# Kernel tuning notes

Measured on AMD Instinct MI355X. Metric: run time of the kernel, lower is better.

Reference implementation:

```python
import jax, jax.numpy as jnp
import numpy as np

B, T, D, I, C, H = 8192, 128, 7, 128, 10, 64
L = 2 ** D
SUBSET = int(I * 0.8)  # feature_subset_size = 102


def setup_inputs() -> dict:
    key = jax.random.key(0)
    ks = jax.random.split(key, 7)
    x = jax.random.normal(ks[0], (B, I), dtype=jnp.float32)
    # exact feature-subset mask: SUBSET ones per (tree, depth) row
    r = jax.random.uniform(ks[1], (T, D, I))
    ranks = jnp.argsort(jnp.argsort(r, axis=-1), axis=-1)
    feature_mask = (ranks < SUBSET).astype(jnp.float32)
    thresholds = jax.random.normal(ks[2], (T, D), dtype=jnp.float32)
    leaf_outputs = jax.random.normal(ks[3], (T, L, C), dtype=jnp.float32)
    W1 = jax.random.normal(ks[4], (I, H), dtype=jnp.float32) * 0.08
    b1 = jnp.zeros((H,), dtype=jnp.float32)
    W2 = jax.random.normal(ks[5], (H, T), dtype=jnp.float32) * 0.12
    b2 = jnp.zeros((T,), dtype=jnp.float32)
    return {"x": x, "feature_mask": feature_mask, "thresholds": thresholds,
            "leaf_outputs": leaf_outputs, "W1": W1, "b1": b1, "W2": W2, "b2": b2}


def reference(x, feature_mask, thresholds, leaf_outputs, W1, b1, W2, b2):
    depth = thresholds.shape[1]
    # split logits: masked feature sum minus threshold, per (batch, tree, depth)
    z = jnp.einsum('bi,tdi->btd', x, feature_mask) - thresholds[None, :, :]
    s = 0.5 * (z / (1.0 + jnp.abs(z)) + 1.0)  # scaled softsign split in (0,1)
    # probabilistic path routing: doubling concat, identical to torch loop
    p = jnp.ones((x.shape[0], feature_mask.shape[0], 1), dtype=x.dtype)
    for d in range(depth):
        sd = s[:, :, d:d + 1]            # [B, T, 1]
        p = jnp.concatenate([p * sd, p * (1.0 - sd)], axis=-1)  # [B, T, 2^(d+1)]
    leaf_probs = jax.nn.softmax(leaf_outputs, axis=-1)           # [T, L, C]
    tree_outputs = jnp.einsum('btl,tlc->btc', p, leaf_probs)     # [B, T, C]
    # instance-wise attention over trees (eval mode: no dropout)
    attn = jax.nn.softmax(jax.nn.relu(x @ W1 + b1) @ W2 + b2, axis=-1)  # [B, T]
    return jnp.sum(tree_outputs * attn[:, :, None], axis=1)     # [B, C]
```

## Files before the change

### kernel.cpp

```cpp
#include <hip/hip_runtime.h>
#include <hip/hip_bf16.h>
#include <hip/hip_fp16.h>


#define BB 8192
#define TT 128
#define II 128
#define CC 10
#define HH 64

#define OFF_SP  0
#define OFF_AT  4194304
#define OFF_LPB 4718592
#define OFF_PT  4980736

typedef __attribute__((ext_vector_type(8))) short short8;
typedef __attribute__((ext_vector_type(16))) float floatx16;

static __device__ inline unsigned int pkbf(float lo, float hi) {
  __hip_bfloat162 h = __float22bfloat162_rn(make_float2(lo, hi));
  unsigned int u;
  __builtin_memcpy(&u, &h, 4);
  return u;
}

static __device__ inline unsigned int pkh(float lo, float hi) {
  __half2 h = __float22half2_rn(make_float2(lo, hi));
  unsigned int u;
  __builtin_memcpy(&u, &h, 4);
  return u;
}

static __device__ inline short8 cvt8(float4 a, float4 b) {
  union { short8 v; unsigned int u[4]; } r;
  r.u[0] = pkbf(a.x, a.y);
  r.u[1] = pkbf(a.z, a.w);
  r.u[2] = pkbf(b.x, b.y);
  r.u[3] = pkbf(b.z, b.w);
  return r.v;
}

__global__ __launch_bounds__(256, 2) void phase1_kernel(
    const float* __restrict__ x, const float* __restrict__ mask,
    const float* __restrict__ thr, const float* __restrict__ lo,
    const float* __restrict__ W1, const float* __restrict__ b1,
    const float* __restrict__ W2, const float* __restrict__ b2,
    __half* __restrict__ sPack, __half* __restrict__ attnB,
    unsigned int* __restrict__ lpb) {
  __shared__ __align__(16) char smem_raw[32768];
  const int blk = blockIdx.x;
  const int tid = threadIdx.x;
  const int wv = tid >> 6, lane = tid & 63;
  const int half = lane >> 5, l31 = lane & 31;

  if (blk < 64) {
    const int b0 = blk * 128 + wv * 32;

    short8 axf[8];
    const float* xrow = x + (size_t)(b0 + l31) * II + half * 8;
#pragma unroll
    for (int s = 0; s < 8; ++s)
      axf[s] = cvt8(*(const float4*)(xrow + s * 16),
                    *(const float4*)(xrow + s * 16 + 4));

    floatx16 acch[2];
#pragma unroll
    for (int i = 0; i < 16; ++i) { acch[0][i] = 0.f; acch[1][i] = 0.f; }
#pragma unroll
    for (int s = 0; s < 8; ++s) {
#pragma unroll
      for (int tile = 0; tile < 2; ++tile) {
        union { short8 v; unsigned int u[4]; } wf;
#pragma unroll
        for (int jp = 0; jp < 4; ++jp) {
          int k0 = s * 16 + half * 8 + jp * 2;
          float f0 = W1[(size_t)k0 * HH + tile * 32 + l31];
          float f1 = W1[(size_t)(k0 + 1) * HH + tile * 32 + l31];
          wf.u[jp] = pkbf(f0, f1);
        }
        acch[tile] = __builtin_amdgcn_mfma_f32_32x32x16_bf16(
            axf[s], wf.v, acch[tile], 0, 0, 0);
      }
    }
    __hip_bfloat16* hids = (__hip_bfloat16*)smem_raw + wv * (32 * 72);
#pragma unroll
    for (int tile = 0; tile < 2; ++tile) {
      float bh = b1[tile * 32 + l31];
#pragma unroll
      for (int r = 0; r < 16; ++r) {
        int row = (r & 3) + 8 * (r >> 2) + 4 * half;
        hids[row * 72 + tile * 32 + l31] =
            __float2bfloat16(fmaxf(acch[tile][r] + bh, 0.f));
      }
    }
    __syncthreads();

    short8 ahf[4];
#pragma unroll
    for (int s = 0; s < 4; ++s)
      ahf[s] = *(const short8*)(hids + l31 * 72 + s * 16 + half * 8);

    floatx16 accl[4];
#pragma unroll
    for (int tile = 0; tile < 4; ++tile) {
#pragma unroll
      for (int i = 0; i < 16; ++i) accl[tile][i] = 0.f;
#pragma unroll
      for (int s = 0; s < 4; ++s) {
        union { short8 v; unsigned int u[4]; } wf;
#pragma unroll
        for (int jp = 0; jp < 4; ++jp) {
          int k0 = s * 16 + half * 8 + jp * 2;
          float f0 = W2[(size_t)k0 * TT + tile * 32 + l31];
          float f1 = W2[(size_t)(k0 + 1) * TT + tile * 32 + l31];
          wf.u[jp] = pkbf(f0, f1);
        }
        accl[tile] = __builtin_amdgcn_mfma_f32_32x32x16_bf16(
            ahf[s], wf.v, accl[tile], 0, 0, 0);
      }
      float bt = b2[tile * 32 + l31];
#pragma unroll
      for (int i = 0; i < 16; ++i) accl[tile][i] += bt;
    }

    float mrow[16];
#pragma unroll
    for (int r = 0; r < 16; ++r)
      mrow[r] = fmaxf(fmaxf(accl[0][r], accl[1][r]),
                      fmaxf(accl[2][r], accl[3][r]));
#pragma unroll
    for (int msk = 1; msk <= 16; msk <<= 1)
#pragma unroll
      for (int r = 0; r < 16; ++r)
        mrow[r] = fmaxf(mrow[r], __shfl_xor(mrow[r], msk, 64));
    float srow[16];
#pragma unroll
    for (int r = 0; r < 16; ++r) srow[r] = 0.f;
#pragma unroll
    for (int tile = 0; tile < 4; ++tile)
#pragma unroll
      for (int r = 0; r < 16; ++r) {
        float e = __expf(accl[tile][r] - mrow[r]);
        accl[tile][r] = e;
        srow[r] += e;
      }
#pragma unroll
    for (int msk = 1; msk <= 16; msk <<= 1)
#pragma unroll
      for (int r = 0; r < 16; ++r)
        srow[r] += __shfl_xor(srow[r], msk, 64);
#pragma unroll
    for (int r = 0; r < 16; ++r) srow[r] = 1.f / srow[r];

#pragma unroll
    for (int tile = 0; tile < 4; ++tile)
#pragma unroll
      for (int r = 0; r < 16; ++r) {
        int row = (r & 3) + 8 * (r >> 2) + 4 * half;
        attnB[(size_t)(b0 + row) * TT + tile * 32 + l31] =
            __float2half(accl[tile][r] * srow[r]);
      }

  } else if (blk < 576) {
    __half* lds = (__half*)smem_raw;
    const int blk2 = blk - 64;
    const int mb = blk2 >> 5;
    const int ns = blk2 & 31;
    const int m0 = mb * 56;

    short8 af0[8], af1[8];
    {
      const float* mrow0 = mask + (size_t)(m0 + l31) * II + half * 8;
      int mr1 = m0 + 28 + l31; if (mr1 > 895) mr1 = 895;
      const float* mrow1 = mask + (size_t)mr1 * II + half * 8;
#pragma unroll
      for (int s = 0; s < 8; ++s) {
        af0[s] = cvt8(*(const float4*)(mrow0 + s * 16),
                      *(const float4*)(mrow0 + s * 16 + 4));
        af1[s] = cvt8(*(const float4*)(mrow1 + s * 16),
                      *(const float4*)(mrow1 + s * 16 + 4));
      }
    }
    float th0[16], th1[16];
#pragma unroll
    for (int r = 0; r < 16; ++r) {
      int rw = (r & 3) + 8 * (r >> 2) + 4 * half;
      th0[r] = thr[m0 + rw];
      int m1 = m0 + 28 + rw;
      th1[r] = thr[m1 > 895 ? 895 : m1];
    }

#pragma unroll
    for (int nb = 0; nb < 2; ++nb) {
      const int nl = wv * 64 + nb * 32;
      const float* xrow = x + (size_t)(ns * 256 + nl + l31) * II + half * 8;
      short8 xf[8];
#pragma unroll
      for (int s = 0; s < 8; ++s)
        xf[s] = cvt8(*(const float4*)(xrow + s * 16),
                     *(const float4*)(xrow + s * 16 + 4));
      floatx16 acc0, acc1;
#pragma unroll
      for (int i = 0; i < 16; ++i) { acc0[i] = 0.f; acc1[i] = 0.f; }
#pragma unroll
      for (int s = 0; s < 8; ++s) {
        acc0 = __builtin_amdgcn_mfma_f32_32x32x16_bf16(af0[s], xf[s], acc0, 0, 0, 0);
        acc1 = __builtin_amdgcn_mfma_f32_32x32x16_bf16(af1[s], xf[s], acc1, 0, 0, 0);
      }
#pragma unroll
      for (int r = 0; r < 16; ++r) {
        int row = (r & 3) + 8 * (r >> 2) + 4 * half;
        if (row < 28) {
          int tl = row / 7;
          int d = row - tl * 7;
          float z = acc0[r] - th0[r];
          float o = 0.5f * (z / (1.f + fabsf(z)) + 1.f);
          lds[(tl * 256 + nl + l31) * 8 + d] = __float2half(o);
          z = acc1[r] - th1[r];
          o = 0.5f * (z / (1.f + fabsf(z)) + 1.f);
          lds[((tl + 4) * 256 + nl + l31) * 8 + d] = __float2half(o);
        }
      }
    }
    __syncthreads();

    const uint4* l4 = (const uint4*)lds;
#pragma unroll
    for (int j = 0; j < 8; ++j) {
      int idx = tid + 256 * j;
      ((uint4*)sPack)[(size_t)(8 * mb + (idx >> 8)) * BB + ns * 256 + (idx & 255)] =
          l4[idx];
    }

  } else {
    float* lps = (float*)smem_raw;
    const int t0 = (blk - 576) * 2;
    {
      int tl = tid >> 7, l = tid & 127;
      const float* row = lo + ((size_t)(t0 + tl) * 128 + l) * CC;
      float v[CC];
      float m = -1e30f;
#pragma unroll
      for (int c = 0; c < CC; ++c) { v[c] = row[c]; m = fmaxf(m, v[c]); }
      float s = 0.f;
#pragma unroll
      for (int c = 0; c < CC; ++c) { v[c] = __expf(v[c] - m); s += v[c]; }
      float inv = 1.f / s;
      float* o = lps + (tl * 128 + l) * 12;
#pragma unroll
      for (int c = 0; c < CC; ++c) o[c] = v[c] * inv;
      o[10] = 0.f; o[11] = 0.f;
    }
    __syncthreads();

#pragma unroll
    for (int jj = 0; jj < 4; ++jj) {
      int idx = tid + 256 * jj;
      int tl = idx >> 9, rem = idx & 511;
      int s = rem >> 6, ln = rem & 63;
      int hf = ln >> 5, n = ln & 31;
      unsigned int wd[4];
#pragma unroll
      for (int jp = 0; jp < 4; ++jp) {
        int l0 = s * 16 + hf * 8 + jp * 2;
        float f0 = (n < CC) ? lps[(tl * 128 + l0) * 12 + n] : 0.f;
        float f1 = (n < CC) ? lps[(tl * 128 + l0 + 1) * 12 + n] : 0.f;
        wd[jp] = pkh(f0, f1);
      }
      ((uint4*)lpb)[(size_t)(t0 + tl) * 512 + s * 64 + ln] =
          make_uint4(wd[0], wd[1], wd[2], wd[3]);
    }
  }
}

__global__ __launch_bounds__(256, 2) void main_kernel(
    const __half* __restrict__ sPack, const __half* __restrict__ attnB,
    const unsigned int* __restrict__ lpb, float* __restrict__ partial) {
  __shared__ float red[256 * 10];
  const int bg = blockIdx.x, tg = blockIdx.y;
  const int tid = threadIdx.x;
  const int w = tid >> 6, lane = tid & 63;
  const int half = lane >> 5;
  const int l31 = lane & 31;
  const int b0 = bg * 256 + w * 64 + l31;
  const int b1 = b0 + 32;
  const uint4* spk = (const uint4*)sPack;

  __half av0[8], av1[8];
  *(uint4*)av0 = *(const uint4*)(attnB + (size_t)b0 * TT + tg * 8);
  *(uint4*)av1 = *(const uint4*)(attnB + (size_t)b1 * TT + tg * 8);

  floatx16 acc0, acc1;
#pragma unroll
  for (int i = 0; i < 16; ++i) { acc0[i] = 0.f; acc1[i] = 0.f; }

  uint4 sv0[2], sv1[2];
  sv0[0] = spk[(size_t)(tg * 8) * BB + b0];
  sv1[0] = spk[(size_t)(tg * 8) * BB + b1];

#pragma unroll
  for (int it = 0; it < 8; ++it) {
    const int cur = it & 1;
    const int t = tg * 8 + it;
    uint4 bf[8];
    const uint4* lpt = (const uint4*)lpb + (size_t)t * 512 + lane;
#pragma unroll
    for (int s = 0; s < 8; ++s) bf[s] = lpt[s * 64];
    if (it < 7) {
      sv0[cur ^ 1] = spk[(size_t)(t + 1) * BB + b0];
      sv1[cur ^ 1] = spk[(size_t)(t + 1) * BB + b1];
    }

    __half2 pl2q[2][4];
    float wvq[2][8];
#pragma unroll
    for (int q = 0; q < 2; ++q) {
      const __half* sh = (const __half*)(q ? &sv1[cur] : &sv0[cur]);
      float s0 = __half2float(sh[0]), s1 = __half2float(sh[1]);
      float s2 = __half2float(sh[2]), s3 = __half2float(sh[3]);
      float s4 = __half2float(sh[4]), s5 = __half2float(sh[5]);
      float s6 = __half2float(sh[6]);
      float A  = __half2float(q ? av1[it] : av0[it]);

      float s0c = 1.f - s0, s1c = 1.f - s1, s2c = 1.f - s2;
      float t0 = s0 * s1, t1 = s0c * s1, t2 = s0 * s1c, t3 = s0c * s1c;
      float pl[8];
      pl[0] = t0 * s2;  pl[1] = t1 * s2;  pl[2] = t2 * s2;  pl[3] = t3 * s2;
      pl[4] = t0 * s2c; pl[5] = t1 * s2c; pl[6] = t2 * s2c; pl[7] = t3 * s2c;
      float sel3 = half ? (1.f - s3) : s3;
      float Af = A * sel3;
      float s4c = 1.f - s4, s5c = 1.f - s5;
      float as6 = Af * s6, as6c = Af * (1.f - s6);
      float u0 = s4 * s5, u1 = s4c * s5, u2 = s4 * s5c, u3 = s4c * s5c;
      wvq[q][0] = u0 * as6;  wvq[q][1] = u1 * as6;
      wvq[q][2] = u2 * as6;  wvq[q][3] = u3 * as6;
      wvq[q][4] = u0 * as6c; wvq[q][5] = u1 * as6c;
      wvq[q][6] = u2 * as6c; wvq[q][7] = u3 * as6c;
#pragma unroll
      for (int jp = 0; jp < 4; ++jp)
        pl2q[q][jp] = __float22half2_rn(make_float2(pl[jp * 2], pl[jp * 2 + 1]));
    }

#pragma unroll
    for (int s = 0; s < 8; ++s) {
      union { short8 v; __half2 h[4]; } a0, a1;
      __half2 w20 = __half2half2(__float2half(wvq[0][s]));
      __half2 w21 = __half2half2(__float2half(wvq[1][s]));
#pragma unroll
      for (int jp = 0; jp < 4; ++jp) {
        a0.h[jp] = __hmul2(pl2q[0][jp], w20);
        a1.h[jp] = __hmul2(pl2q[1][jp], w21);
      }
      acc0 = __builtin_amdgcn_mfma_f32_32x32x16_f16(
          a0.v, *(const short8*)&bf[s], acc0, 0, 0, 0);
      acc1 = __builtin_amdgcn_mfma_f32_32x32x16_f16(
          a1.v, *(const short8*)&bf[s], acc1, 0, 0, 0);
    }
  }

  const int col = l31;
  if (col < CC) {
#pragma unroll
    for (int r = 0; r < 16; ++r) {
      int row = (r & 3) + 8 * (r >> 2) + 4 * half;
      red[(w * 64 + row) * 10 + col] = acc0[r];
      red[(w * 64 + 32 + row) * 10 + col] = acc1[r];
    }
  }
  __syncthreads();
#pragma unroll
  for (int j = 0; j < 10; ++j) {
    int idx = tid + 256 * j;
    partial[(size_t)tg * 81920 + (size_t)bg * 2560 + idx] = red[idx];
  }
}

__global__ __launch_bounds__(256) void reduce_kernel(
    const float* __restrict__ partial, float* __restrict__ out) {
  int idx4 = blockIdx.x * 256 + threadIdx.x;
  float4 s = make_float4(0.f, 0.f, 0.f, 0.f);
#pragma unroll
  for (int tg = 0; tg < 16; ++tg) {
    float4 v = ((const float4*)(partial + (size_t)tg * 81920))[idx4];
    s.x += v.x; s.y += v.y; s.z += v.z; s.w += v.w;
  }
  ((float4*)out)[idx4] = s;
}

extern "C" void kernel_launch(void* const* d_in, const int* in_sizes, int n_in,
                              void* d_out, int out_size, void* d_ws, size_t ws_size,
                              hipStream_t stream) {
  const float* x    = (const float*)d_in[0];
  const float* mask = (const float*)d_in[1];
  const float* thr  = (const float*)d_in[2];
  const float* lo   = (const float*)d_in[3];
  const float* W1   = (const float*)d_in[4];
  const float* b1   = (const float*)d_in[5];
  const float* W2   = (const float*)d_in[6];
  const float* b2   = (const float*)d_in[7];
  float* out = (float*)d_out;
  float* ws  = (float*)d_ws;

  __half*       sPack   = (__half*)(ws + OFF_SP);
  __half*       attnB   = (__half*)(ws + OFF_AT);
  unsigned int* LPb     = (unsigned int*)(ws + OFF_LPB);
  float*        partial = ws + OFF_PT;

  phase1_kernel<<<640, 256, 0, stream>>>(x, mask, thr, lo, W1, b1, W2, b2,
                                         sPack, attnB, LPb);
  main_kernel<<<dim3(32, 16), 256, 0, stream>>>(sPack, attnB, LPb, partial);
  reduce_kernel<<<80, 256, 0, stream>>>(partial, out);
}
```

Baseline: 105.5 us.

## Fuse split, attention, leaf-softmax and routing into one kernel with atomic reduction

Replaces the three-kernel pipeline (phase1, main, reduce) with a single fused kernel. Each block computes its split probabilities, its slice of attention and its leaf softmaxes in LDS, then runs the routing MFMA and atomically adds its partial result into the output, which is zeroed first with a memset. This removes the workspace round trips through global memory and two kernel launches. In exchange, every block recomputes the attention MLP for its 256 rows, so that work is repeated 16 times across tree groups. LDS use also grows to about 62KB per block, which may limit occupancy, and results depend on atomic add order.

```diff
diff --git a/kernel.cpp b/kernel.cpp
--- a/kernel.cpp
+++ b/kernel.cpp
@@ -8,11 +8,6 @@
 #define II 128
 #define CC 10
 #define HH 64
-
-#define OFF_SP  0
-#define OFF_AT  4194304
-#define OFF_LPB 4718592
-#define OFF_PT  4980736
 
 typedef __attribute__((ext_vector_type(8))) short short8;
 typedef __attribute__((ext_vector_type(16))) float floatx16;
@@ -40,134 +35,23 @@
   return r.v;
 }
 
-__global__ __launch_bounds__(256, 2) void phase1_kernel(
+__global__ __launch_bounds__(256, 2) void fused_kernel(
     const float* __restrict__ x, const float* __restrict__ mask,
     const float* __restrict__ thr, const float* __restrict__ lo,
     const float* __restrict__ W1, const float* __restrict__ b1,
     const float* __restrict__ W2, const float* __restrict__ b2,
-    __half* __restrict__ sPack, __half* __restrict__ attnB,
-    unsigned int* __restrict__ lpb) {
-  __shared__ __align__(16) char smem_raw[32768];
-  const int blk = blockIdx.x;
+    float* __restrict__ out) {
+  __shared__ __align__(16) char smem_raw[63488];
   const int tid = threadIdx.x;
   const int wv = tid >> 6, lane = tid & 63;
   const int half = lane >> 5, l31 = lane & 31;
-
-  if (blk < 64) {
-    const int b0 = blk * 128 + wv * 32;
-
-    short8 axf[8];
-    const float* xrow = x + (size_t)(b0 + l31) * II + half * 8;
-#pragma unroll
-    for (int s = 0; s < 8; ++s)
-      axf[s] = cvt8(*(const float4*)(xrow + s * 16),
-                    *(const float4*)(xrow + s * 16 + 4));
-
-    floatx16 acch[2];
-#pragma unroll
-    for (int i = 0; i < 16; ++i) { acch[0][i] = 0.f; acch[1][i] = 0.f; }
-#pragma unroll
-    for (int s = 0; s < 8; ++s) {
-#pragma unroll
-      for (int tile = 0; tile < 2; ++tile) {
-        union { short8 v; unsigned int u[4]; } wf;
-#pragma unroll
-        for (int jp = 0; jp < 4; ++jp) {
-          int k0 = s * 16 + half * 8 + jp * 2;
-          float f0 = W1[(size_t)k0 * HH + tile * 32 + l31];
-          float f1 = W1[(size_t)(k0 + 1) * HH + tile * 32 + l31];
-          wf.u[jp] = pkbf(f0, f1);
-        }
-        acch[tile] = __builtin_amdgcn_mfma_f32_32x32x16_bf16(
-            axf[s], wf.v, acch[tile], 0, 0, 0);
-      }
-    }
-    __hip_bfloat16* hids = (__hip_bfloat16*)smem_raw + wv * (32 * 72);
-#pragma unroll
-    for (int tile = 0; tile < 2; ++tile) {
-      float bh = b1[tile * 32 + l31];
-#pragma unroll
-      for (int r = 0; r < 16; ++r) {
-        int row = (r & 3) + 8 * (r >> 2) + 4 * half;
-        hids[row * 72 + tile * 32 + l31] =
-            __float2bfloat16(fmaxf(acch[tile][r] + bh, 0.f));
-      }
-    }
-    __syncthreads();
-
-    short8 ahf[4];
-#pragma unroll
-    for (int s = 0; s < 4; ++s)
-      ahf[s] = *(const short8*)(hids + l31 * 72 + s * 16 + half * 8);
-
-    floatx16 accl[4];
-#pragma unroll
-    for (int tile = 0; tile < 4; ++tile) {
-#pragma unroll
-      for (int i = 0; i < 16; ++i) accl[tile][i] = 0.f;
-#pragma unroll
-      for (int s = 0; s < 4; ++s) {
-        union { short8 v; unsigned int u[4]; } wf;
-#pragma unroll
-        for (int jp = 0; jp < 4; ++jp) {
-          int k0 = s * 16 + half * 8 + jp * 2;
-          float f0 = W2[(size_t)k0 * TT + tile * 32 + l31];
-          float f1 = W2[(size_t)(k0 + 1) * TT + tile * 32 + l31];
-          wf.u[jp] = pkbf(f0, f1);
-        }
-        accl[tile] = __builtin_amdgcn_mfma_f32_32x32x16_bf16(
-            ahf[s], wf.v, accl[tile], 0, 0, 0);
-      }
-      float bt = b2[tile * 32 + l31];
-#pragma unroll
-      for (int i = 0; i < 16; ++i) accl[tile][i] += bt;
-    }
-
-    float mrow[16];
-#pragma unroll
-    for (int r = 0; r < 16; ++r)
-      mrow[r] = fmaxf(fmaxf(accl[0][r], accl[1][r]),
-                      fmaxf(accl[2][r], accl[3][r]));
-#pragma unroll
-    for (int msk = 1; msk <= 16; msk <<= 1)
-#pragma unroll
-      for (int r = 0; r < 16; ++r)
-        mrow[r] = fmaxf(mrow[r], __shfl_xor(mrow[r], msk, 64));
-    float srow[16];
-#pragma unroll
-    for (int r = 0; r < 16; ++r) srow[r] = 0.f;
-#pragma unroll
-    for (int tile = 0; tile < 4; ++tile)
-#pragma unroll
-      for (int r = 0; r < 16; ++r) {
-        float e = __expf(accl[tile][r] - mrow[r]);
-        accl[tile][r] = e;
-        srow[r] += e;
-      }
-#pragma unroll
-    for (int msk = 1; msk <= 16; msk <<= 1)
-#pragma unroll
-      for (int r = 0; r < 16; ++r)
-        srow[r] += __shfl_xor(srow[r], msk, 64);
-#pragma unroll
-    for (int r = 0; r < 16; ++r) srow[r] = 1.f / srow[r];
-
-#pragma unroll
-    for (int tile = 0; tile < 4; ++tile)
-#pragma unroll
-      for (int r = 0; r < 16; ++r) {
-        int row = (r & 3) + 8 * (r >> 2) + 4 * half;
-        attnB[(size_t)(b0 + row) * TT + tile * 32 + l31] =
-            __float2half(accl[tile][r] * srow[r]);
-      }
-
-  } else if (blk < 576) {
-    __half* lds = (__half*)smem_raw;
-    const int blk2 = blk - 64;
-    const int mb = blk2 >> 5;
-    const int ns = blk2 & 31;
-    const int m0 = mb * 56;
-
+  const int tg = blockIdx.x >> 5;
+  const int bg = blockIdx.x & 31;
+
+  __half* zsl = (__half*)smem_raw;
+
+  {
+    const int m0 = tg * 56;
     short8 af0[8], af1[8];
     {
       const float* mrow0 = mask + (size_t)(m0 + l31) * II + half * 8;
@@ -193,7 +77,7 @@
 #pragma unroll
     for (int nb = 0; nb < 2; ++nb) {
       const int nl = wv * 64 + nb * 32;
-      const float* xrow = x + (size_t)(ns * 256 + nl + l31) * II + half * 8;
+      const float* xrow = x + (size_t)(bg * 256 + nl + l31) * II + half * 8;
       short8 xf[8];
 #pragma unroll
       for (int s = 0; s < 8; ++s)
@@ -215,176 +99,264 @@
           int d = row - tl * 7;
           float z = acc0[r] - th0[r];
           float o = 0.5f * (z / (1.f + fabsf(z)) + 1.f);
-          lds[(tl * 256 + nl + l31) * 8 + d] = __float2half(o);
+          zsl[(tl * 256 + nl + l31) * 8 + d] = __float2half(o);
           z = acc1[r] - th1[r];
           o = 0.5f * (z / (1.f + fabsf(z)) + 1.f);
-          lds[((tl + 4) * 256 + nl + l31) * 8 + d] = __float2half(o);
-        }
-      }
-    }
+          zsl[((tl + 4) * 256 + nl + l31) * 8 + d] = __float2half(o);
+        }
+      }
+    }
+  }
+
+  {
+    const int tsel = tg >> 2, lsel = tg & 3;
+    __half* attnV = (__half*)(smem_raw + 59392);
+    for (int p = 0; p < 2; ++p) {
+      const int b0 = bg * 256 + p * 128 + wv * 32;
+
+      short8 axf[8];
+      const float* xrow = x + (size_t)(b0 + l31) * II + half * 8;
+#pragma unroll
+      for (int s = 0; s < 8; ++s)
+        axf[s] = cvt8(*(const float4*)(xrow + s * 16),
+                      *(const float4*)(xrow + s * 16 + 4));
+
+      floatx16 acch[2];
+#pragma unroll
+      for (int i = 0; i < 16; ++i) { acch[0][i] = 0.f; acch[1][i] = 0.f; }
+#pragma unroll
+      for (int s = 0; s < 8; ++s) {
+#pragma unroll
+        for (int tile = 0; tile < 2; ++tile) {
+          union { short8 v; unsigned int u[4]; } wf;
+#pragma unroll
+          for (int jp = 0; jp < 4; ++jp) {
+            int k0 = s * 16 + half * 8 + jp * 2;
+            float f0 = W1[(size_t)k0 * HH + tile * 32 + l31];
+            float f1 = W1[(size_t)(k0 + 1) * HH + tile * 32 + l31];
+            wf.u[jp] = pkbf(f0, f1);
+          }
+          acch[tile] = __builtin_amdgcn_mfma_f32_32x32x16_bf16(
+              axf[s], wf.v, acch[tile], 0, 0, 0);
+        }
+      }
+      __hip_bfloat16* hids = (__hip_bfloat16*)(smem_raw + 32768) + wv * (32 * 72);
+#pragma unroll
+      for (int tile = 0; tile < 2; ++tile) {
+        float bh = b1[tile * 32 + l31];
+#pragma unroll
+        for (int r = 0; r < 16; ++r) {
+          int row = (r & 3) + 8 * (r >> 2) + 4 * half;
+          hids[row * 72 + tile * 32 + l31] =
+              __float2bfloat16(fmaxf(acch[tile][r] + bh, 0.f));
+        }
+      }
+      __syncthreads();
+
+      short8 ahf[4];
+#pragma unroll
+      for (int s = 0; s < 4; ++s)
+        ahf[s] = *(const short8*)(hids + l31 * 72 + s * 16 + half * 8);
+
+      floatx16 accl[4];
+#pragma unroll
+      for (int tile = 0; tile < 4; ++tile) {
+#pragma unroll
+        for (int i = 0; i < 16; ++i) accl[tile][i] = 0.f;
+#pragma unroll
+        for (int s = 0; s < 4; ++s) {
+          union { short8 v; unsigned int u[4]; } wf;
+#pragma unroll
+          for (int jp = 0; jp < 4; ++jp) {
+            int k0 = s * 16 + half * 8 + jp * 2;
+            float f0 = W2[(size_t)k0 * TT + tile * 32 + l31];
+            float f1 = W2[(size_t)(k0 + 1) * TT + tile * 32 + l31];
+            wf.u[jp] = pkbf(f0, f1);
+          }
+          accl[tile] = __builtin_amdgcn_mfma_f32_32x32x16_bf16(
+              ahf[s], wf.v, accl[tile], 0, 0, 0);
+        }
+        float bt = b2[tile * 32 + l31];
+#pragma unroll
+        for (int i = 0; i < 16; ++i) accl[tile][i] += bt;
+      }
+
+      float mrow[16];
+#pragma unroll
+      for (int r = 0; r < 16; ++r)
+        mrow[r] = fmaxf(fmaxf(accl[0][r], accl[1][r]),
+                        fmaxf(accl[2][r], accl[3][r]));
+#pragma unroll
+      for (int msk = 1; msk <= 16; msk <<= 1)
+#pragma unroll
+        for (int r = 0; r < 16; ++r)
+          mrow[r] = fmaxf(mrow[r], __shfl_xor(mrow[r], msk, 64));
+      float srow[16];
+#pragma unroll
+      for (int r = 0; r < 16; ++r) srow[r] = 0.f;
+#pragma unroll
+      for (int tile = 0; tile < 4; ++tile)
+#pragma unroll
+        for (int r = 0; r < 16; ++r) {
+          float e = __expf(accl[tile][r] - mrow[r]);
+          accl[tile][r] = e;
+          srow[r] += e;
+        }
+#pragma unroll
+      for (int msk = 1; msk <= 16; msk <<= 1)
+#pragma unroll
+        for (int r = 0; r < 16; ++r)
+          srow[r] += __shfl_xor(srow[r], msk, 64);
+#pragma unroll
+      for (int r = 0; r < 16; ++r) srow[r] = 1.f / srow[r];
+
+#pragma unroll
+      for (int tile = 0; tile < 4; ++tile) {
+        if (tile == tsel) {
+#pragma unroll
+          for (int r = 0; r < 16; ++r) {
+            int row = (r & 3) + 8 * (r >> 2) + 4 * half;
+            if ((l31 >> 3) == lsel)
+              attnV[(p * 128 + wv * 32 + row) * 8 + (l31 & 7)] =
+                  __float2half(accl[tile][r] * srow[r]);
+          }
+        }
+      }
+      __syncthreads();
+    }
+  }
+
+  {
+    __half* lps = (__half*)(smem_raw + 53248);
+    uint4* lpB = (uint4*)(smem_raw + 32768);
+    for (int tt = 0; tt < 4; ++tt) {
+      {
+        int tl = tid >> 7, l = tid & 127;
+        const float* row = lo + ((size_t)(tg * 8 + tt * 2 + tl) * 128 + l) * CC;
+        float v[CC];
+        float m = -1e30f;
+#pragma unroll
+        for (int c = 0; c < CC; ++c) { v[c] = row[c]; m = fmaxf(m, v[c]); }
+        float s = 0.f;
+#pragma unroll
+        for (int c = 0; c < CC; ++c) { v[c] = __expf(v[c] - m); s += v[c]; }
+        float inv = 1.f / s;
+        __half* o = lps + (tl * 128 + l) * 12;
+#pragma unroll
+        for (int c = 0; c < CC; ++c) o[c] = __float2half(v[c] * inv);
+      }
+      __syncthreads();
+#pragma unroll
+      for (int jj = 0; jj < 4; ++jj) {
+        int idx = tid + 256 * jj;
+        int tl = idx >> 9, rem = idx & 511;
+        int s = rem >> 6, ln = rem & 63;
+        int hf = ln >> 5, n = ln & 31;
+        if (n < CC) {
+          unsigned int wd[4];
+#pragma unroll
+          for (int jp = 0; jp < 4; ++jp) {
+            int l0 = s * 16 + hf * 8 + jp * 2;
+            float f0 = __half2float(lps[(tl * 128 + l0) * 12 + n]);
+            float f1 = __half2float(lps[(tl * 128 + l0 + 1) * 12 + n]);
+            wd[jp] = pkh(f0, f1);
+          }
+          lpB[((tt * 2 + tl) * 8 + s) * 20 + n * 2 + hf] =
+              make_uint4(wd[0], wd[1], wd[2], wd[3]);
+        }
+      }
+      __syncthreads();
+    }
+  }
+
+  {
+    const uint4* zsl4 = (const uint4*)smem_raw;
+    const uint4* lpB = (const uint4*)(smem_raw + 32768);
+    const uint4* aV = (const uint4*)(smem_raw + 59392);
+    const int bl = wv * 64 + l31;
+
+    __half av0[8], av1[8];
+    *(uint4*)av0 = aV[bl];
+    *(uint4*)av1 = aV[bl + 32];
+
+    floatx16 acc0, acc1;
+#pragma unroll
+    for (int i = 0; i < 16; ++i) { acc0[i] = 0.f; acc1[i] = 0.f; }
+
+#pragma unroll
+    for (int it = 0; it < 8; ++it) {
+      uint4 sv0 = zsl4[it * 256 + bl];
+      uint4 sv1 = zsl4[it * 256 + bl + 32];
+      uint4 bf[8];
+#pragma unroll
+      for (int s = 0; s < 8; ++s)
+        bf[s] = (l31 < CC) ? lpB[(it * 8 + s) * 20 + l31 * 2 + half]
+                           : make_uint4(0u, 0u, 0u, 0u);
+
+      __half2 pl2q[2][4];
+      float wvq[2][8];
+#pragma unroll
+      for (int q = 0; q < 2; ++q) {
+        const __half* sh = (const __half*)(q ? &sv1 : &sv0);
+        float s0 = __half2float(sh[0]), s1 = __half2float(sh[1]);
+        float s2 = __half2float(sh[2]), s3 = __half2float(sh[3]);
+        float s4 = __half2float(sh[4]), s5 = __half2float(sh[5]);
+        float s6 = __half2float(sh[6]);
+        float A  = __half2float(q ? av1[it] : av0[it]);
+
+        float s0c = 1.f - s0, s1c = 1.f - s1, s2c = 1.f - s2;
+        float t0 = s0 * s1, t1 = s0c * s1, t2 = s0 * s1c, t3 = s0c * s1c;
+        float pl[8];
+        pl[0] = t0 * s2;  pl[1] = t1 * s2;  pl[2] = t2 * s2;  pl[3] = t3 * s2;
+        pl[4] = t0 * s2c; pl[5] = t1 * s2c; pl[6] = t2 * s2c; pl[7] = t3 * s2c;
+        float sel3 = half ? (1.f - s3) : s3;
+        float Af = A * sel3;
+        float s4c = 1.f - s4, s5c = 1.f - s5;
+        float as6 = Af * s6, as6c = Af * (1.f - s6);
+        float u0 = s4 * s5, u1 = s4c * s5, u2 = s4 * s5c, u3 = s4c * s5c;
+        wvq[q][0] = u0 * as6;  wvq[q][1] = u1 * as6;
+        wvq[q][2] = u2 * as6;  wvq[q][3] = u3 * as6;
+        wvq[q][4] = u0 * as6c; wvq[q][5] = u1 * as6c;
+        wvq[q][6] = u2 * as6c; wvq[q][7] = u3 * as6c;
+#pragma unroll
+        for (int jp = 0; jp < 4; ++jp)
+          pl2q[q][jp] = __float22half2_rn(make_float2(pl[jp * 2], pl[jp * 2 + 1]));
+      }
+
+#pragma unroll
+      for (int s = 0; s < 8; ++s) {
+        union { short8 v; __half2 h[4]; } a0, a1;
+        __half2 w20 = __half2half2(__float2half(wvq[0][s]));
+        __half2 w21 = __half2half2(__float2half(wvq[1][s]));
+#pragma unroll
+        for (int jp = 0; jp < 4; ++jp) {
+          a0.h[jp] = __hmul2(pl2q[0][jp], w20);
+          a1.h[jp] = __hmul2(pl2q[1][jp], w21);
+        }
+        acc0 = __builtin_amdgcn_mfma_f32_32x32x16_f16(
+            a0.v, *(const short8*)&bf[s], acc0, 0, 0, 0);
+        acc1 = __builtin_amdgcn_mfma_f32_32x32x16_f16(
+            a1.v, *(const short8*)&bf[s], acc1, 0, 0, 0);
+      }
+    }
+
     __syncthreads();
-
-    const uint4* l4 = (const uint4*)lds;
-#pragma unroll
-    for (int j = 0; j < 8; ++j) {
+    float* red = (float*)(smem_raw + 32768);
+    if (l31 < CC) {
+#pragma unroll
+      for (int r = 0; r < 16; ++r) {
+        int row = (r & 3) + 8 * (r >> 2) + 4 * half;
+        red[(wv * 64 + row) * 10 + l31] = acc0[r];
+        red[(wv * 64 + 32 + row) * 10 + l31] = acc1[r];
+      }
+    }
+    __syncthreads();
+#pragma unroll
+    for (int j = 0; j < 10; ++j) {
       int idx = tid + 256 * j;
-      ((uint4*)sPack)[(size_t)(8 * mb + (idx >> 8)) * BB + ns * 256 + (idx & 255)] =
-          l4[idx];
-    }
-
-  } else {
-    float* lps = (float*)smem_raw;
-    const int t0 = (blk - 576) * 2;
-    {
-      int tl = tid >> 7, l = tid & 127;
-      const float* row = lo + ((size_t)(t0 + tl) * 128 + l) * CC;
-      float v[CC];
-      float m = -1e30f;
-#pragma unroll
-      for (int c = 0; c < CC; ++c) { v[c] = row[c]; m = fmaxf(m, v[c]); }
-      float s = 0.f;
-#pragma unroll
-      for (int c = 0; c < CC; ++c) { v[c] = __expf(v[c] - m); s += v[c]; }
-      float inv = 1.f / s;
-      float* o = lps + (tl * 128 + l) * 12;
-#pragma unroll
-      for (int c = 0; c < CC; ++c) o[c] = v[c] * inv;
-      o[10] = 0.f; o[11] = 0.f;
-    }
-    __syncthreads();
-
-#pragma unroll
-    for (int jj = 0; jj < 4; ++jj) {
-      int idx = tid + 256 * jj;
-      int tl = idx >> 9, rem = idx & 511;
-      int s = rem >> 6, ln = rem & 63;
-      int hf = ln >> 5, n = ln & 31;
-      unsigned int wd[4];
-#pragma unroll
-      for (int jp = 0; jp < 4; ++jp) {
-        int l0 = s * 16 + hf * 8 + jp * 2;
-        float f0 = (n < CC) ? lps[(tl * 128 + l0) * 12 + n] : 0.f;
-        float f1 = (n < CC) ? lps[(tl * 128 + l0 + 1) * 12 + n] : 0.f;
-        wd[jp] = pkh(f0, f1);
-      }
-      ((uint4*)lpb)[(size_t)(t0 + tl) * 512 + s * 64 + ln] =
-          make_uint4(wd[0], wd[1], wd[2], wd[3]);
+      atomicAdd(out + (size_t)bg * 2560 + idx, red[idx]);
     }
   }
-}
-
-__global__ __launch_bounds__(256, 2) void main_kernel(
-    const __half* __restrict__ sPack, const __half* __restrict__ attnB,
-    const unsigned int* __restrict__ lpb, float* __restrict__ partial) {
-  __shared__ float red[256 * 10];
-  const int bg = blockIdx.x, tg = blockIdx.y;
-  const int tid = threadIdx.x;
-  const int w = tid >> 6, lane = tid & 63;
-  const int half = lane >> 5;
-  const int l31 = lane & 31;
-  const int b0 = bg * 256 + w * 64 + l31;
-  const int b1 = b0 + 32;
-  const uint4* spk = (const uint4*)sPack;
-
-  __half av0[8], av1[8];
-  *(uint4*)av0 = *(const uint4*)(attnB + (size_t)b0 * TT + tg * 8);
-  *(uint4*)av1 = *(const uint4*)(attnB + (size_t)b1 * TT + tg * 8);
-
-  floatx16 acc0, acc1;
-#pragma unroll
-  for (int i = 0; i < 16; ++i) { acc0[i] = 0.f; acc1[i] = 0.f; }
-
-  uint4 sv0[2], sv1[2];
-  sv0[0] = spk[(size_t)(tg * 8) * BB + b0];
-  sv1[0] = spk[(size_t)(tg * 8) * BB + b1];
-
-#pragma unroll
-  for (int it = 0; it < 8; ++it) {
-    const int cur = it & 1;
-    const int t = tg * 8 + it;
-    uint4 bf[8];
-    const uint4* lpt = (const uint4*)lpb + (size_t)t * 512 + lane;
-#pragma unroll
-    for (int s = 0; s < 8; ++s) bf[s] = lpt[s * 64];
-    if (it < 7) {
-      sv0[cur ^ 1] = spk[(size_t)(t + 1) * BB + b0];
-      sv1[cur ^ 1] = spk[(size_t)(t + 1) * BB + b1];
-    }
-
-    __half2 pl2q[2][4];
-    float wvq[2][8];
-#pragma unroll
-    for (int q = 0; q < 2; ++q) {
-      const __half* sh = (const __half*)(q ? &sv1[cur] : &sv0[cur]);
-      float s0 = __half2float(sh[0]), s1 = __half2float(sh[1]);
-      float s2 = __half2float(sh[2]), s3 = __half2float(sh[3]);
-      float s4 = __half2float(sh[4]), s5 = __half2float(sh[5]);
-      float s6 = __half2float(sh[6]);
-      float A  = __half2float(q ? av1[it] : av0[it]);
-
-      float s0c = 1.f - s0, s1c = 1.f - s1, s2c = 1.f - s2;
-      float t0 = s0 * s1, t1 = s0c * s1, t2 = s0 * s1c, t3 = s0c * s1c;
-      float pl[8];
-      pl[0] = t0 * s2;  pl[1] = t1 * s2;  pl[2] = t2 * s2;  pl[3] = t3 * s2;
-      pl[4] = t0 * s2c; pl[5] = t1 * s2c; pl[6] = t2 * s2c; pl[7] = t3 * s2c;
-      float sel3 = half ? (1.f - s3) : s3;
-      float Af = A * sel3;
-      float s4c = 1.f - s4, s5c = 1.f - s5;
-      float as6 = Af * s6, as6c = Af * (1.f - s6);
-      float u0 = s4 * s5, u1 = s4c * s5, u2 = s4 * s5c, u3 = s4c * s5c;
-      wvq[q][0] = u0 * as6;  wvq[q][1] = u1 * as6;
-      wvq[q][2] = u2 * as6;  wvq[q][3] = u3 * as6;
-      wvq[q][4] = u0 * as6c; wvq[q][5] = u1 * as6c;
-      wvq[q][6] = u2 * as6c; wvq[q][7] = u3 * as6c;
-#pragma unroll
-      for (int jp = 0; jp < 4; ++jp)
-        pl2q[q][jp] = __float22half2_rn(make_float2(pl[jp * 2], pl[jp * 2 + 1]));
-    }
-
-#pragma unroll
-    for (int s = 0; s < 8; ++s) {
-      union { short8 v; __half2 h[4]; } a0, a1;
-      __half2 w20 = __half2half2(__float2half(wvq[0][s]));
-      __half2 w21 = __half2half2(__float2half(wvq[1][s]));
-#pragma unroll
-      for (int jp = 0; jp < 4; ++jp) {
-        a0.h[jp] = __hmul2(pl2q[0][jp], w20);
-        a1.h[jp] = __hmul2(pl2q[1][jp], w21);
-      }
-      acc0 = __builtin_amdgcn_mfma_f32_32x32x16_f16(
-          a0.v, *(const short8*)&bf[s], acc0, 0, 0, 0);
-      acc1 = __builtin_amdgcn_mfma_f32_32x32x16_f16(
-          a1.v, *(const short8*)&bf[s], acc1, 0, 0, 0);
-    }
-  }
-
-  const int col = l31;
-  if (col < CC) {
-#pragma unroll
-    for (int r = 0; r < 16; ++r) {
-      int row = (r & 3) + 8 * (r >> 2) + 4 * half;
-      red[(w * 64 + row) * 10 + col] = acc0[r];
-      red[(w * 64 + 32 + row) * 10 + col] = acc1[r];
-    }
-  }
-  __syncthreads();
-#pragma unroll
-  for (int j = 0; j < 10; ++j) {
-    int idx = tid + 256 * j;
-    partial[(size_t)tg * 81920 + (size_t)bg * 2560 + idx] = red[idx];
-  }
-}
-
-__global__ __launch_bounds__(256) void reduce_kernel(
-    const float* __restrict__ partial, float* __restrict__ out) {
-  int idx4 = blockIdx.x * 256 + threadIdx.x;
-  float4 s = make_float4(0.f, 0.f, 0.f, 0.f);
-#pragma unroll
-  for (int tg = 0; tg < 16; ++tg) {
-    float4 v = ((const float4*)(partial + (size_t)tg * 81920))[idx4];
-    s.x += v.x; s.y += v.y; s.z += v.z; s.w += v.w;
-  }
-  ((float4*)out)[idx4] = s;
 }
 
 extern "C" void kernel_launch(void* const* d_in, const int* in_sizes, int n_in,
@@ -399,15 +371,7 @@
   const float* W2   = (const float*)d_in[6];
   const float* b2   = (const float*)d_in[7];
   float* out = (float*)d_out;
-  float* ws  = (float*)d_ws;
-
-  __half*       sPack   = (__half*)(ws + OFF_SP);
-  __half*       attnB   = (__half*)(ws + OFF_AT);
-  unsigned int* LPb     = (unsigned int*)(ws + OFF_LPB);
-  float*        partial = ws + OFF_PT;
-
-  phase1_kernel<<<640, 256, 0, stream>>>(x, mask, thr, lo, W1, b1, W2, b2,
-                                         sPack, attnB, LPb);
-  main_kernel<<<dim3(32, 16), 256, 0, stream>>>(sPack, attnB, LPb, partial);
-  reduce_kernel<<<80, 256, 0, stream>>>(partial, out);
-}
+
+  hipMemsetAsync(out, 0, (size_t)out_size * sizeof(float), stream);
+  fused_kernel<<<512, 256, 0, stream>>>(x, mask, thr, lo, W1, b1, W2, b2, out);
+}
```

After: 120.5 us. +14.2%, slower.
